# Performance work log

Hardware: AMD Instinct MI355X
Metric: run time of the kernel (lower is better)

The kernel has to match this reference:

```python
import jax, jax.numpy as jnp
import numpy as np

N_EMBED = 768
NUM_HEADS = 12
HEAD_SIZE = N_EMBED // NUM_HEADS
EPS = 1e-6


def layer_norm(x, gamma, beta):
    # torch .var() is unbiased (ddof=1)
    mean = x.mean(-1, keepdims=True)
    var = jnp.var(x, axis=-1, keepdims=True, ddof=1)
    xhat = (x - mean) / jnp.sqrt(var + EPS)
    return gamma * xhat + beta


def setup_inputs() -> dict:
    key = jax.random.key(0)
    ks = jax.random.split(key, 10)
    B, S, D = 4, 2048, N_EMBED
    H = 4 * D
    s = 0.02
    return {
        "x": jax.random.normal(ks[0], (B, S, D), jnp.float32),
        "wq": jax.random.normal(ks[1], (D, D), jnp.float32) * s,
        "wk": jax.random.normal(ks[2], (D, D), jnp.float32) * s,
        "wv": jax.random.normal(ks[3], (D, D), jnp.float32) * s,
        "wo": jax.random.normal(ks[4], (D, D), jnp.float32) * s,
        "w1": jax.random.normal(ks[5], (D, H), jnp.float32) * s,
        "b1": jnp.zeros((H,), jnp.float32),
        "w2": jax.random.normal(ks[6], (H, D), jnp.float32) * s,
        "b2": jnp.zeros((D,), jnp.float32),
        "gamma1": jnp.ones((D,), jnp.float32),
        "beta1": jnp.zeros((D,), jnp.float32),
        "gamma2": jnp.ones((D,), jnp.float32),
        "beta2": jnp.zeros((D,), jnp.float32),
    }


def reference(x, wq, wk, wv, wo, w1, b1, w2, b2, gamma1, beta1, gamma2, beta2):
    B, S, D = x.shape
    Hh, hs = NUM_HEADS, HEAD_SIZE

    # --- pre-LN causal self-attention ---
    xn = layer_norm(x, gamma1, beta1)
    q = (xn @ wq).reshape(B, S, Hh, hs).transpose(0, 2, 1, 3)  # [B,H,S,hs]
    k = (xn @ wk).reshape(B, S, Hh, hs).transpose(0, 2, 1, 3)
    v = (xn @ wv).reshape(B, S, Hh, hs).transpose(0, 2, 1, 3)

    scale = 1.0 / np.sqrt(hs).astype(np.float32)
    scores = jnp.einsum("bhqd,bhkd->bhqk", q, k) * scale  # [B,H,S,S]
    causal = jnp.tril(jnp.ones((S, S), bool))
    scores = jnp.where(causal, scores, -jnp.inf)
    weights = jax.nn.softmax(scores, axis=-1)
    attn = jnp.einsum("bhqk,bhkd->bhqd", weights, v)  # [B,H,S,hs]
    attn = attn.transpose(0, 2, 1, 3).reshape(B, S, D)
    x = x + attn @ wo

    # --- pre-LN MLP ---
    xn = layer_norm(x, gamma2, beta2)
    h = jax.nn.relu(xn @ w1 + b1)
    x = x + (h @ w2 + b2)
    return x
```

## Files before the change

### kernel.cpp

```cpp
#include <hip/hip_runtime.h>
#include <hip/hip_bf16.h>
#include <math.h>

#define BATCH 4
#define SEQ   2048
#define DMODEL 768
#define NHEAD 12
#define HS    64
#define HID   3072
#define NROWS (BATCH*SEQ)
#define QKVN  (3*DMODEL)
#define EPS   1e-6f

typedef __attribute__((ext_vector_type(8))) short bf16x8;
typedef __attribute__((ext_vector_type(4))) float f32x4;

__device__ inline ushort f2b(float f) {
    union { float f; unsigned u; } x; x.f = f;
    unsigned u = x.u;
    unsigned r = (u + 0x7FFFu + ((u >> 16) & 1u)) >> 16;
    return (ushort)r;
}

#define GLDS16(g, l) __builtin_amdgcn_global_load_lds( \
    (const __attribute__((address_space(1))) void*)(g), \
    (__attribute__((address_space(3))) void*)(l), 16, 0, 0)

__global__ __launch_bounds__(256) void convert_w4(const float* __restrict__ p0,
                                                  const float* __restrict__ p1,
                                                  const float* __restrict__ p2,
                                                  const float* __restrict__ p3,
                                                  ushort* __restrict__ out) {
    const float* srcs[4] = { p0, p1, p2, p3 };
    const float* in = srcs[blockIdx.z];
    ushort* dst = out + (size_t)blockIdx.z * DMODEL * DMODEL;
    __shared__ float tile[32][33];
    const int bx = blockIdx.x * 32;
    const int by = blockIdx.y * 32;
    const int tx = threadIdx.x & 31, ty = threadIdx.x >> 5;
    #pragma unroll
    for (int i = 0; i < 32; i += 8)
        tile[ty + i][tx] = in[(size_t)(by + ty + i) * DMODEL + bx + tx];
    __syncthreads();
    #pragma unroll
    for (int i = 0; i < 32; i += 8)
        dst[(size_t)(bx + ty + i) * DMODEL + by + tx] = f2b(tile[tx][ty + i]);
}

__global__ __launch_bounds__(256) void convert_w(const float* __restrict__ in,
                                                 ushort* __restrict__ out,
                                                 int K, int N) {
    __shared__ float tile[32][33];
    const int bx = blockIdx.x * 32;
    const int by = blockIdx.y * 32;
    const int tx = threadIdx.x & 31, ty = threadIdx.x >> 5;
    #pragma unroll
    for (int i = 0; i < 32; i += 8)
        tile[ty + i][tx] = in[(size_t)(by + ty + i) * N + bx + tx];
    __syncthreads();
    #pragma unroll
    for (int i = 0; i < 32; i += 8)
        out[(size_t)(bx + ty + i) * K + by + tx] = f2b(tile[tx][ty + i]);
}

__global__ __launch_bounds__(256) void transpose_v(const ushort* __restrict__ v,
                                                   ushort* __restrict__ vt) {
    const int st = blockIdx.x;
    const int bh = blockIdx.y;
    const int b = bh / NHEAD, h = bh % NHEAD;
    const ushort* src = v + ((size_t)b * SEQ) * QKVN + h * HS;
    ushort* dst = vt + ((size_t)bh * HS) * SEQ;
    __shared__ ushort t[64][65];
    const int col = threadIdx.x & 63;
    const int r0  = (threadIdx.x >> 6) * 16;
    #pragma unroll
    for (int i = 0; i < 16; ++i)
        t[col][r0 + i] = src[(size_t)(st * 64 + r0 + i) * QKVN + col];
    __syncthreads();
    #pragma unroll
    for (int i = 0; i < 16; ++i)
        dst[(size_t)(r0 + i) * SEQ + st * 64 + col] = t[r0 + i][col];
}

__global__ __launch_bounds__(256) void ln_kernel(const float* __restrict__ x,
                                                 const float* __restrict__ gamma,
                                                 const float* __restrict__ beta,
                                                 ushort* __restrict__ out) {
    const int row = blockIdx.x;
    const float* xr = x + (size_t)row * DMODEL;
    float s = 0.f, s2 = 0.f;
    for (int i = threadIdx.x; i < DMODEL; i += 256) {
        float v = xr[i];
        s += v; s2 += v * v;
    }
    for (int off = 32; off > 0; off >>= 1) {
        s  += __shfl_down(s,  off, 64);
        s2 += __shfl_down(s2, off, 64);
    }
    __shared__ float shs[4], shs2[4];
    int wid = threadIdx.x >> 6, lane = threadIdx.x & 63;
    if (lane == 0) { shs[wid] = s; shs2[wid] = s2; }
    __syncthreads();
    __shared__ float smean, srstd;
    if (threadIdx.x == 0) {
        float S  = shs[0] + shs[1] + shs[2] + shs[3];
        float S2 = shs2[0] + shs2[1] + shs2[2] + shs2[3];
        float mean = S / DMODEL;
        float var  = (S2 - DMODEL * mean * mean) / (DMODEL - 1);
        smean = mean;
        srstd = rsqrtf(var + EPS);
    }
    __syncthreads();
    float mean = smean, rstd = srstd;
    ushort* orow = out + (size_t)row * DMODEL;
    for (int i = threadIdx.x; i < DMODEL; i += 256) {
        orow[i] = f2b(gamma[i] * (xr[i] - mean) * rstd + beta[i]);
    }
}

#define GN 128
#define GK 64
#define GM 64
__global__ __launch_bounds__(256, 3) void gemm_mfma(const ushort* __restrict__ A,
                                                    const ushort* __restrict__ Bt,
                                                    const float* __restrict__ bias,
                                                    const float* __restrict__ res,
                                                    float* __restrict__ C,
                                                    ushort* __restrict__ Cb,
                                                    int M, int N, int K, int do_relu,
                                                    int scale_q) {
    __shared__ ushort As[2][GM * GK];
    __shared__ ushort Bs[2][GN * GK];
    const int tid  = threadIdx.x;
    const int lane = tid & 63, wave = tid >> 6;
    const int l16  = lane & 15, quad = lane >> 4;
    const int wr = wave >> 1, wc = wave & 1;

    const int nwg = gridDim.x * gridDim.y;
    int id = blockIdx.y * gridDim.x + blockIdx.x;
    if ((nwg & 7) == 0) {
        const int chunk = nwg >> 3;
        id = (id & 7) * chunk + (id >> 3);
    }
    const int bx = id % gridDim.x;
    const int by = id / gridDim.x;
    const int row0 = by * GM, col0 = bx * GN;

    f32x4 acc[2][4];
    #pragma unroll
    for (int i = 0; i < 2; ++i)
        #pragma unroll
        for (int j = 0; j < 4; ++j) acc[i][j] = (f32x4){0.f, 0.f, 0.f, 0.f};

    const ushort* Asrc[2];
    const ushort* Bsrc[4];
    #pragma unroll
    for (int i = 0; i < 2; ++i) {
        int c = tid + i * 256, m = c >> 3, j = c & 7;
        Asrc[i] = A + (size_t)(row0 + m) * K + (j ^ (m & 7)) * 8;
    }
    #pragma unroll
    for (int i = 0; i < 4; ++i) {
        int c = tid + i * 256, m = c >> 3, j = c & 7;
        Bsrc[i] = Bt + (size_t)(col0 + m) * K + (j ^ (m & 7)) * 8;
    }

    const int nk = K / GK;
    #pragma unroll
    for (int i = 0; i < 2; ++i) GLDS16(Asrc[i], &As[0][(tid + i * 256) * 8]);
    #pragma unroll
    for (int i = 0; i < 4; ++i)  GLDS16(Bsrc[i], &Bs[0][(tid + i * 256) * 8]);

    for (int kt = 0; kt < nk; ++kt) {
        const int p = kt & 1;
        __syncthreads();
        if (kt + 1 < nk) {
            const int k1 = (kt + 1) * GK;
            #pragma unroll
            for (int i = 0; i < 2; ++i) GLDS16(Asrc[i] + k1, &As[p ^ 1][(tid + i * 256) * 8]);
            #pragma unroll
            for (int i = 0; i < 4; ++i)  GLDS16(Bsrc[i] + k1, &Bs[p ^ 1][(tid + i * 256) * 8]);
        }

        #pragma unroll
        for (int s = 0; s < 2; ++s) {
            bf16x8 af[2], bfr[4];
            #pragma unroll
            for (int i = 0; i < 2; ++i) {
                int m = wr * 32 + i * 16 + l16;
                af[i] = *(const bf16x8*)&As[p][(m * 8 + (((s << 2) | quad) ^ (m & 7))) * 8];
            }
            #pragma unroll
            for (int j = 0; j < 4; ++j) {
                int n = wc * 64 + j * 16 + l16;
                bfr[j] = *(const bf16x8*)&Bs[p][(n * 8 + (((s << 2) | quad) ^ (n & 7))) * 8];
            }
            #pragma unroll
            for (int i = 0; i < 2; ++i)
                #pragma unroll
                for (int j = 0; j < 4; ++j)
                    acc[i][j] = __builtin_amdgcn_mfma_f32_16x16x32_bf16(af[i], bfr[j], acc[i][j], 0, 0, 0);
        }
    }

    #pragma unroll
    for (int i = 0; i < 2; ++i) {
        #pragma unroll
        for (int r = 0; r < 4; ++r) {
            int row = row0 + wr * 32 + i * 16 + quad * 4 + r;
            #pragma unroll
            for (int j = 0; j < 4; ++j) {
                int col = col0 + wc * 64 + j * 16 + l16;
                float v = acc[i][j][r];
                if (bias) v += bias[col];
                if (do_relu) v = fmaxf(v, 0.f);
                if (scale_q && col < DMODEL) v *= 0.125f;
                if (res) v += res[(size_t)row * N + col];
                if (Cb) Cb[(size_t)row * N + col] = f2b(v);
                else    C [(size_t)row * N + col] = v;
            }
        }
    }
}

#define HM 128
#define HN 128
#define HK 32
__global__ __launch_bounds__(256, 4) void gemm_big(const ushort* __restrict__ A,
                                                   const ushort* __restrict__ Bt,
                                                   const float* __restrict__ bias,
                                                   const float* __restrict__ res,
                                                   float* __restrict__ C,
                                                   ushort* __restrict__ Cb,
                                                   int M, int N, int K, int do_relu,
                                                   int scale_q) {
    __shared__ ushort As[2][HM * HK];
    __shared__ ushort Bs[2][HN * HK];
    const int tid  = threadIdx.x;
    const int lane = tid & 63, wave = tid >> 6;
    const int l16  = lane & 15, quad = lane >> 4;
    const int wr = wave >> 1, wc = wave & 1;

    const int nwg = gridDim.x * gridDim.y;
    int id = blockIdx.y * gridDim.x + blockIdx.x;
    if ((nwg & 7) == 0) {
        const int chunk = nwg >> 3;
        id = (id & 7) * chunk + (id >> 3);
    }
    const int bx = id % gridDim.x;
    const int by = id / gridDim.x;
    const int row0 = by * HM, col0 = bx * HN;

    f32x4 acc[4][4];
    #pragma unroll
    for (int i = 0; i < 4; ++i)
        #pragma unroll
        for (int j = 0; j < 4; ++j) acc[i][j] = (f32x4){0.f, 0.f, 0.f, 0.f};

    const ushort* Asrc[2];
    const ushort* Bsrc[2];
    #pragma unroll
    for (int i = 0; i < 2; ++i) {
        int c = tid + i * 256;
        int lr = c >> 3, pp = (c & 7) ^ (lr & 7);
        int m = lr * 2 + (pp >> 2), j = pp & 3;
        Asrc[i] = A  + (size_t)(row0 + m) * K + j * 8;
        Bsrc[i] = Bt + (size_t)(col0 + m) * K + j * 8;
    }

    const int nk = K / HK;
    #pragma unroll
    for (int i = 0; i < 2; ++i) GLDS16(Asrc[i], &As[0][(tid + i * 256) * 8]);
    #pragma unroll
    for (int i = 0; i < 2; ++i) GLDS16(Bsrc[i], &Bs[0][(tid + i * 256) * 8]);

    for (int kt = 0; kt < nk; ++kt) {
        const int p = kt & 1;
        __syncthreads();
        if (kt + 1 < nk) {
            const int k1 = (kt + 1) * HK;
            #pragma unroll
            for (int i = 0; i < 2; ++i) GLDS16(Asrc[i] + k1, &As[p ^ 1][(tid + i * 256) * 8]);
            #pragma unroll
            for (int i = 0; i < 2; ++i) GLDS16(Bsrc[i] + k1, &Bs[p ^ 1][(tid + i * 256) * 8]);
        }

        bf16x8 af[4], bfr[4];
        #pragma unroll
        for (int i = 0; i < 4; ++i) {
            int m = wr * 64 + i * 16 + l16;
            int ch = (m >> 1) * 8 + ((((m & 1) << 2) | quad) ^ ((m >> 1) & 7));
            af[i] = *(const bf16x8*)&As[p][ch * 8];
        }
        #pragma unroll
        for (int j = 0; j < 4; ++j) {
            int n = wc * 64 + j * 16 + l16;
            int ch = (n >> 1) * 8 + ((((n & 1) << 2) | quad) ^ ((n >> 1) & 7));
            bfr[j] = *(const bf16x8*)&Bs[p][ch * 8];
        }
        #pragma unroll
        for (int i = 0; i < 4; ++i)
            #pragma unroll
            for (int j = 0; j < 4; ++j)
                acc[i][j] = __builtin_amdgcn_mfma_f32_16x16x32_bf16(af[i], bfr[j], acc[i][j], 0, 0, 0);
    }

    #pragma unroll
    for (int i = 0; i < 4; ++i) {
        #pragma unroll
        for (int r = 0; r < 4; ++r) {
            int row = row0 + wr * 64 + i * 16 + quad * 4 + r;
            #pragma unroll
            for (int j = 0; j < 4; ++j) {
                int col = col0 + wc * 64 + j * 16 + l16;
                float v = acc[i][j][r];
                if (bias) v += bias[col];
                if (do_relu) v = fmaxf(v, 0.f);
                if (scale_q && col < DMODEL) v *= 0.125f;
                if (res) v += res[(size_t)row * N + col];
                if (Cb) Cb[(size_t)row * N + col] = f2b(v);
                else    C [(size_t)row * N + col] = v;
            }
        }
    }
}

#define TQ 64
#define TK 64
#define PPAD 72
#define NQT (SEQ / TQ)

__global__ __launch_bounds__(256, 3) void fattn_kernel(const ushort* __restrict__ q,
                                                       const ushort* __restrict__ k,
                                                       const ushort* __restrict__ vt,
                                                       ushort* __restrict__ o,
                                                       int ldqkv) {
    const int pair = blockIdx.x;
    const int qts[2] = { pair, NQT - 1 - pair };
    const int bh = blockIdx.y;
    const int b = bh / NHEAD, h = bh % NHEAD;
    const int tid  = threadIdx.x;
    const int wave = tid >> 6;
    const int lane = tid & 63;
    const int l16  = lane & 15;
    const int quad = lane >> 4;

    __shared__ ushort Ks[2][TK * 64];
    __shared__ ushort Vs[2][HS * 64];
    __shared__ ushort Ps[4][16][PPAD];

    const size_t base  = ((size_t)b * SEQ) * ldqkv + (size_t)h * HS;
    const size_t baseO = ((size_t)b * SEQ) * DMODEL + (size_t)h * HS;
    const ushort* vth = vt + ((size_t)bh * HS) * SEQ;

    const int r0 = tid >> 3, j0 = (tid & 7) ^ (r0 & 7);
    const int r1 = (tid + 256) >> 3, j1 = (tid & 7) ^ (r1 & 7);
    const ushort* Ksrc0 = k + base + (size_t)r0 * ldqkv + j0 * 8;
    const ushort* Ksrc1 = k + base + (size_t)r1 * ldqkv + j1 * 8;
    const ushort* Vsrc0 = vth + (size_t)r0 * SEQ + j0 * 8;
    const ushort* Vsrc1 = vth + (size_t)r1 * SEQ + j1 * 8;

    bf16x8 qf[2][2];
    #pragma unroll
    for (int t = 0; t < 2; ++t) {
        int qrow = qts[t] * TQ + wave * 16 + l16;
        const ushort* qp = q + base + (size_t)qrow * ldqkv + quad * 8;
        qf[t][0] = *(const bf16x8*)(qp);
        qf[t][1] = *(const bf16x8*)(qp + 32);
    }

    f32x4 Oacc[2][4];
    float lrow[2][4];
    #pragma unroll
    for (int t = 0; t < 2; ++t) {
        #pragma unroll
        for (int f = 0; f < 4; ++f) Oacc[t][f] = (f32x4){0.f, 0.f, 0.f, 0.f};
        #pragma unroll
        for (int r = 0; r < 4; ++r) lrow[t][r] = 0.f;
    }

    const int ktiles = qts[1] + 1;
    GLDS16(Ksrc0, &Ks[0][tid * 8]);
    GLDS16(Ksrc1, &Ks[0][(tid + 256) * 8]);
    GLDS16(Vsrc0, &Vs[0][tid * 8]);
    GLDS16(Vsrc1, &Vs[0][(tid + 256) * 8]);

    for (int kt = 0; kt < ktiles; ++kt) {
        const int p = kt & 1;
        __syncthreads();
        if (kt + 1 < ktiles) {
            const size_t ko = (size_t)(kt + 1) * TK;
            GLDS16(Ksrc0 + ko * ldqkv, &Ks[p ^ 1][tid * 8]);
            GLDS16(Ksrc1 + ko * ldqkv, &Ks[p ^ 1][(tid + 256) * 8]);
            GLDS16(Vsrc0 + ko,         &Vs[p ^ 1][tid * 8]);
            GLDS16(Vsrc1 + ko,         &Vs[p ^ 1][(tid + 256) * 8]);
        }

        bf16x8 kb[4][2], vb[4][2];
        #pragma unroll
        for (int f = 0; f < 4; ++f) {
            int row = f * 16 + l16;
            kb[f][0] = *(const bf16x8*)&Ks[p][(row * 8 + (quad ^ (row & 7))) * 8];
            kb[f][1] = *(const bf16x8*)&Ks[p][(row * 8 + ((4 | quad) ^ (row & 7))) * 8];
            vb[f][0] = *(const bf16x8*)&Vs[p][(row * 8 + (quad ^ (row & 7))) * 8];
            vb[f][1] = *(const bf16x8*)&Vs[p][(row * 8 + ((4 | quad) ^ (row & 7))) * 8];
        }

        #pragma unroll
        for (int t = 0; t < 2; ++t) {
            const int qt = qts[t];
            if (kt > qt) continue;

            f32x4 S[4];
            #pragma unroll
            for (int f = 0; f < 4; ++f) {
                f32x4 a = (f32x4){0.f, 0.f, 0.f, 0.f};
                a = __builtin_amdgcn_mfma_f32_16x16x32_bf16(qf[t][0], kb[f][0], a, 0, 0, 0);
                a = __builtin_amdgcn_mfma_f32_16x16x32_bf16(qf[t][1], kb[f][1], a, 0, 0, 0);
                S[f] = a;
            }

            const int qrow_base = qt * TQ + wave * 16 + quad * 4;
            if (kt == qt) {
                #pragma unroll
                for (int f = 0; f < 4; ++f) {
                    int key = kt * TK + f * 16 + l16;
                    #pragma unroll
                    for (int r = 0; r < 4; ++r)
                        if (key > qrow_base + r) S[f][r] = -INFINITY;
                }
            }

            #pragma unroll
            for (int f = 0; f < 4; ++f) {
                #pragma unroll
                for (int r = 0; r < 4; ++r) {
                    float pv = __expf(S[f][r]);
                    S[f][r] = pv;
                    lrow[t][r] += pv;
                }
            }

            #pragma unroll
            for (int f = 0; f < 4; ++f)
                #pragma unroll
                for (int r = 0; r < 4; ++r)
                    Ps[wave][quad * 4 + r][f * 16 + l16] = f2b(S[f][r]);

            bf16x8 pa0 = *(const bf16x8*)&Ps[wave][l16][quad * 8];
            bf16x8 pa1 = *(const bf16x8*)&Ps[wave][l16][32 + quad * 8];
            #pragma unroll
            for (int f = 0; f < 4; ++f) {
                Oacc[t][f] = __builtin_amdgcn_mfma_f32_16x16x32_bf16(pa0, vb[f][0], Oacc[t][f], 0, 0, 0);
                Oacc[t][f] = __builtin_amdgcn_mfma_f32_16x16x32_bf16(pa1, vb[f][1], Oacc[t][f], 0, 0, 0);
            }
        }
    }

    #pragma unroll
    for (int t = 0; t < 2; ++t) {
        const int qrow = qts[t] * TQ + wave * 16 + quad * 4;
        #pragma unroll
        for (int r = 0; r < 4; ++r) {
            float l = lrow[t][r];
            #pragma unroll
            for (int m = 1; m < 16; m <<= 1) l += __shfl_xor(l, m, 64);
            float invl = 1.f / l;
            #pragma unroll
            for (int f = 0; f < 4; ++f)
                o[baseO + (size_t)(qrow + r) * DMODEL + f * 16 + l16] = f2b(Oacc[t][f][r] * invl);
        }
    }
}

extern "C" void kernel_launch(void* const* d_in, const int* in_sizes, int n_in,
                              void* d_out, int out_size, void* d_ws, size_t ws_size,
                              hipStream_t stream) {
    const float* x      = (const float*)d_in[0];
    const float* wq     = (const float*)d_in[1];
    const float* wk     = (const float*)d_in[2];
    const float* wv     = (const float*)d_in[3];
    const float* wo     = (const float*)d_in[4];
    const float* w1     = (const float*)d_in[5];
    const float* b1     = (const float*)d_in[6];
    const float* w2     = (const float*)d_in[7];
    const float* b2     = (const float*)d_in[8];
    const float* gamma1 = (const float*)d_in[9];
    const float* beta1  = (const float*)d_in[10];
    const float* gamma2 = (const float*)d_in[11];
    const float* beta2  = (const float*)d_in[12];
    float* out = (float*)d_out;

    char* ws = (char*)d_ws;
    ushort* buf_xn   = (ushort*)ws;
    ushort* buf_attn = buf_xn;
    ushort* buf_qkv  = (ushort*)(ws + 12582912);
    ushort* buf_h    = buf_qkv;
    ushort* w_qkv    = (ushort*)(ws + 12582912 + 50331648);
    ushort* w_ot     = w_qkv + (size_t)QKVN * DMODEL;
    ushort* w_1t     = w_ot + (size_t)DMODEL * DMODEL;
    ushort* w_2t     = w_1t + (size_t)HID * DMODEL;
    ushort* buf_vt   = (ushort*)d_out;

    convert_w4<<<dim3(DMODEL/32, DMODEL/32, 4), 256, 0, stream>>>(wq, wk, wv, wo, w_qkv);
    convert_w<<<dim3(HID/32,    DMODEL/32), 256, 0, stream>>>(w1, w_1t, DMODEL, HID);
    convert_w<<<dim3(DMODEL/32, HID/32),    256, 0, stream>>>(w2, w_2t, HID, DMODEL);

    ln_kernel<<<NROWS, 256, 0, stream>>>(x, gamma1, beta1, buf_xn);
    gemm_big<<<dim3(QKVN/HN, NROWS/HM), 256, 0, stream>>>(buf_xn, w_qkv, nullptr, nullptr,
                                                          nullptr, buf_qkv, NROWS, QKVN, DMODEL, 0, 1);
    transpose_v<<<dim3(SEQ/64, BATCH*NHEAD), 256, 0, stream>>>(buf_qkv + 2*DMODEL, buf_vt);
    fattn_kernel<<<dim3(NQT/2, BATCH*NHEAD), 256, 0, stream>>>(buf_qkv, buf_qkv + DMODEL,
                                                               buf_vt, buf_attn, QKVN);
    gemm_mfma<<<dim3(DMODEL/GN, NROWS/GM), 256, 0, stream>>>(buf_attn, w_ot, nullptr, x,
                                                             out, nullptr, NROWS, DMODEL, DMODEL, 0, 0);
    ln_kernel<<<NROWS, 256, 0, stream>>>(out, gamma2, beta2, buf_xn);
    gemm_big<<<dim3(HID/HN, NROWS/HM), 256, 0, stream>>>(buf_xn, w_1t, b1, nullptr,
                                                         nullptr, buf_h, NROWS, HID, DMODEL, 1, 0);
    gemm_mfma<<<dim3(DMODEL/GN, NROWS/GM), 256, 0, stream>>>(buf_h, w_2t, b2, out,
                                                             out, nullptr, NROWS, DMODEL, HID, 0, 0);
}
```

Before: 412.8 us.

## Triple-buffer LDS in gemm_big with explicit vmcnt waits for deeper prefetch

Switches the large GEMM kernel from double to triple buffering of the A/B shared-memory tiles. Loads are issued two k-steps ahead, and a partial s_waitcnt vmcnt(4) lets the next tile's loads stay in flight while the current tile is consumed, which is meant to hide more global-load latency behind the MFMAs. The cost is 50% more LDS per block, and launch bounds drop from 4 to 3 blocks per CU, so occupancy may fall.

```diff
diff --git a/kernel.cpp b/kernel.cpp
--- a/kernel.cpp
+++ b/kernel.cpp
@@ -226,7 +226,7 @@
 #define HM 128
 #define HN 128
 #define HK 32
-__global__ __launch_bounds__(256, 4) void gemm_big(const ushort* __restrict__ A,
+__global__ __launch_bounds__(256, 3) void gemm_big(const ushort* __restrict__ A,
                                                    const ushort* __restrict__ Bt,
                                                    const float* __restrict__ bias,
                                                    const float* __restrict__ res,
@@ -234,8 +234,8 @@
                                                    ushort* __restrict__ Cb,
                                                    int M, int N, int K, int do_relu,
                                                    int scale_q) {
-    __shared__ ushort As[2][HM * HK];
-    __shared__ ushort Bs[2][HN * HK];
+    __shared__ ushort As[3][HM * HK];
+    __shared__ ushort Bs[3][HN * HK];
     const int tid  = threadIdx.x;
     const int lane = tid & 63, wave = tid >> 6;
     const int l16  = lane & 15, quad = lane >> 4;
@@ -269,40 +269,45 @@
     }
 
     const int nk = K / HK;
-    #pragma unroll
-    for (int i = 0; i < 2; ++i) GLDS16(Asrc[i], &As[0][(tid + i * 256) * 8]);
-    #pragma unroll
-    for (int i = 0; i < 2; ++i) GLDS16(Bsrc[i], &Bs[0][(tid + i * 256) * 8]);
-
-    for (int kt = 0; kt < nk; ++kt) {
-        const int p = kt & 1;
-        __syncthreads();
-        if (kt + 1 < nk) {
-            const int k1 = (kt + 1) * HK;
-            #pragma unroll
-            for (int i = 0; i < 2; ++i) GLDS16(Asrc[i] + k1, &As[p ^ 1][(tid + i * 256) * 8]);
-            #pragma unroll
-            for (int i = 0; i < 2; ++i) GLDS16(Bsrc[i] + k1, &Bs[p ^ 1][(tid + i * 256) * 8]);
-        }
+
+#define STAGE_BIG(kt, b) do { \
+    const int _k = (kt) * HK; \
+    GLDS16(Asrc[0] + _k, &As[b][tid * 8]); \
+    GLDS16(Asrc[1] + _k, &As[b][(tid + 256) * 8]); \
+    GLDS16(Bsrc[0] + _k, &Bs[b][tid * 8]); \
+    GLDS16(Bsrc[1] + _k, &Bs[b][(tid + 256) * 8]); \
+} while (0)
+
+    STAGE_BIG(0, 0);
+    STAGE_BIG(1, 1);
+
+    int pc = 0, pn = 1, ps = 2;
+    for (int t = 0; t < nk; ++t) {
+        if (t + 1 < nk) asm volatile("s_waitcnt vmcnt(4)" ::: "memory");
+        else            asm volatile("s_waitcnt vmcnt(0)" ::: "memory");
+        __builtin_amdgcn_s_barrier();
+        if (t + 2 < nk) STAGE_BIG(t + 2, ps);
 
         bf16x8 af[4], bfr[4];
         #pragma unroll
         for (int i = 0; i < 4; ++i) {
             int m = wr * 64 + i * 16 + l16;
             int ch = (m >> 1) * 8 + ((((m & 1) << 2) | quad) ^ ((m >> 1) & 7));
-            af[i] = *(const bf16x8*)&As[p][ch * 8];
+            af[i] = *(const bf16x8*)&As[pc][ch * 8];
         }
         #pragma unroll
         for (int j = 0; j < 4; ++j) {
             int n = wc * 64 + j * 16 + l16;
             int ch = (n >> 1) * 8 + ((((n & 1) << 2) | quad) ^ ((n >> 1) & 7));
-            bfr[j] = *(const bf16x8*)&Bs[p][ch * 8];
+            bfr[j] = *(const bf16x8*)&Bs[pc][ch * 8];
         }
         #pragma unroll
         for (int i = 0; i < 4; ++i)
             #pragma unroll
             for (int j = 0; j < 4; ++j)
                 acc[i][j] = __builtin_amdgcn_mfma_f32_16x16x32_bf16(af[i], bfr[j], acc[i][j], 0, 0, 0);
+
+        int tmp = pc; pc = pn; pn = ps; ps = tmp;
     }
 
     #pragma unroll
```

Result: no change. 419.8 us (+1.7%).
